# Kernel optimization log

Measured on AMD Instinct MI355X. Metric: run time of the kernel, lower is better.

The kernel has to match this reference:

```python
import jax, jax.numpy as jnp
import numpy as np

G_NUMS = 30      # group_nums
G_SIZE = 100     # group_size (also neighborhood_size)
BETA = 1.0
EPS = 1e-9


def setup_inputs() -> dict:
    key = jax.random.key(0)
    pointclouds = jax.random.normal(key, (8, 131072, 3), dtype=jnp.float32)
    return {"pointclouds": pointclouds}


def _knn_gather(points, queries, k):
    """points [b,N,3], queries [b,G,3] -> k nearest points per query [b,G,k,3]."""
    # squared distances [b,G,N]
    d2 = (
        jnp.sum(queries * queries, axis=-1)[..., None]
        - 2.0 * jnp.einsum("bgd,bnd->bgn", queries, points)
        + jnp.sum(points * points, axis=-1)[:, None, :]
    )
    _, idx = jax.lax.top_k(-d2, k)                    # [b,G,k]
    nbrs = jax.vmap(lambda p, i: p[i])(points, idx)   # [b,G,k,3]
    return nbrs


def reference(pointclouds):
    b, N, _ = pointclouds.shape
    # --- group_points: uniform-stride sampled centers, k-NN groups, group means ---
    stride = N // G_NUMS
    centers = pointclouds[:, ::stride][:, :G_NUMS]                 # [b,G,3]
    grouped = _knn_gather(pointclouds, centers, G_SIZE)            # [b,G,K,3]
    group_means = jnp.mean(grouped, axis=2)                        # [b,G,3]

    # --- estimate_pointcloud_local_coord_frames: per-group 3x3 PCA ---
    nbrs = _knn_gather(pointclouds, group_means, G_SIZE)           # [b,G,K,3]
    mu = jnp.mean(nbrs, axis=2, keepdims=True)
    X = nbrs - mu
    cov = jnp.einsum("bgkd,bgke->bgde", X, X) / G_SIZE             # [b,G,3,3]
    curvatures, frames = jnp.linalg.eigh(cov)                      # eigvals ascending

    # --- elongated-shape loss ---
    denom = curvatures[..., 0] + curvatures[..., 1] + curvatures[..., 2] + EPS
    first_vec = curvatures[..., 2] / denom
    second_vec = curvatures[..., 1] / denom
    elongated_shape_loss = -jnp.sum(first_vec - second_vec) / b

    # --- angular smoothness cost over group means / principal directions ---
    dirs = frames[..., :, 2]                                       # [b,G,3] largest-eig direction
    dm = jnp.sum(
        (group_means[:, :, None, :] - group_means[:, None, :, :]) ** 2, axis=-1
    )                                                              # [b,G,G]
    dm = dm + jnp.eye(G_NUMS, dtype=dm.dtype) * jnp.float32(1e30)  # exclude self
    j = jnp.argmin(dm, axis=-1)                                    # [b,G]
    dirs_j = jnp.take_along_axis(dirs, j[..., None], axis=1)       # [b,G,3]
    cos = jnp.sum(dirs * dirs_j, axis=-1)
    dlo_smooth_loss = jnp.mean(1.0 - cos * cos)                    # sign-invariant angle cost

    return elongated_shape_loss + BETA * dlo_smooth_loss
```

## Files before the change

### kernel.cpp

```cpp
#include <hip/hip_runtime.h>
#include <math.h>

#define N_PTS     131072
#define G_NUMS    30
#define G_SIZE    100
#define PT_STRIDE (N_PTS / G_NUMS)
#define TPB       512
#define NWAVES    (TPB / 64)
#define BINS      4096
#define SHIFT     20
#define SAMPLE_GRPS 1024
#define RANK_CUT  32
#define CAP       3072
#define TIE_CAP   64

struct KSmem {
    unsigned hist[BINS];
    unsigned wsum[NWAVES];
    unsigned T;
    int ns, nd, nt;
    unsigned u[CAP];
    int idx[CAP];
    int sel[G_SIZE];
    unsigned tu[TIE_CAP];
    int ti[TIE_CAP];
    float acc[3];
    float cov[6];
    float q[3];
    unsigned tau0;
    unsigned maxu;
    unsigned r1;
    float delta2;
    int fastok;
};

__device__ __forceinline__ float dist2f(float px, float py, float pz,
                                        float qx, float qy, float qz) {
    float dx = px - qx, dy = py - qy, dz = pz - qz;
    return fmaf(dx, dx, fmaf(dy, dy, dz * dz));
}

__device__ __forceinline__ unsigned find_bin(KSmem& sm, unsigned rank,
                                             int tid, int lane, int wid) {
    unsigned hv[8], csum = 0;
#pragma unroll
    for (int j = 0; j < 8; j++) { hv[j] = sm.hist[tid * 8 + j]; csum += hv[j]; }
    unsigned inc = csum;
#pragma unroll
    for (int off = 1; off < 64; off <<= 1) {
        unsigned n = __shfl_up(inc, off);
        if (lane >= off) inc += n;
    }
    __syncthreads();
    if (lane == 63) sm.wsum[wid] = inc;
    __syncthreads();
    unsigned base = 0;
    for (int w = 0; w < wid; w++) base += sm.wsum[w];
    unsigned c = base + inc - csum;
#pragma unroll
    for (int j = 0; j < 8; j++) {
        if (c < rank && c + hv[j] >= rank) sm.T = (unsigned)(tid * 8 + j);
        c += hv[j];
    }
    __syncthreads();
    return sm.T;
}

template<bool SOA>
__device__ __forceinline__ void load_pt(const float* __restrict__ P,
                                        const float* __restrict__ BX,
                                        const float* __restrict__ BY,
                                        const float* __restrict__ BZ,
                                        int idx, float& x, float& y, float& z) {
    if constexpr (SOA) {
        x = BX[idx]; y = BY[idx]; z = BZ[idx];
    } else {
        const float* pp = P + 3 * (size_t)idx;
        x = pp[0]; y = pp[1]; z = pp[2];
    }
}

template<bool SOA>
__device__ void full_select(const float4* __restrict__ P4,
                            const float4* __restrict__ X4,
                            const float4* __restrict__ Y4,
                            const float4* __restrict__ Z4,
                            KSmem& sm, float qx, float qy, float qz,
                            int tid, int lane, int wid, bool save_tau) {
    for (int j = tid; j < BINS; j += TPB) sm.hist[j] = 0u;
    if (tid == 0) { sm.ns = 0; sm.nd = 0; sm.nt = 0; sm.T = 0u; }
    __syncthreads();

    if constexpr (SOA) {
        for (int i = tid; i < SAMPLE_GRPS; i += TPB) {
            float4 xv = X4[i], yv = Y4[i], zv = Z4[i];
            atomicAdd(&sm.hist[__float_as_uint(dist2f(xv.x, yv.x, zv.x, qx, qy, qz)) >> SHIFT], 1u);
            atomicAdd(&sm.hist[__float_as_uint(dist2f(xv.y, yv.y, zv.y, qx, qy, qz)) >> SHIFT], 1u);
            atomicAdd(&sm.hist[__float_as_uint(dist2f(xv.z, yv.z, zv.z, qx, qy, qz)) >> SHIFT], 1u);
            atomicAdd(&sm.hist[__float_as_uint(dist2f(xv.w, yv.w, zv.w, qx, qy, qz)) >> SHIFT], 1u);
        }
    } else {
        for (int grp = tid; grp < SAMPLE_GRPS; grp += TPB) {
            float4 f0 = P4[3 * grp + 0];
            float4 f1 = P4[3 * grp + 1];
            float4 f2 = P4[3 * grp + 2];
            atomicAdd(&sm.hist[__float_as_uint(dist2f(f0.x, f0.y, f0.z, qx, qy, qz)) >> SHIFT], 1u);
            atomicAdd(&sm.hist[__float_as_uint(dist2f(f0.w, f1.x, f1.y, qx, qy, qz)) >> SHIFT], 1u);
            atomicAdd(&sm.hist[__float_as_uint(dist2f(f1.z, f1.w, f2.x, qx, qy, qz)) >> SHIFT], 1u);
            atomicAdd(&sm.hist[__float_as_uint(dist2f(f2.y, f2.z, f2.w, qx, qy, qz)) >> SHIFT], 1u);
        }
    }
    __syncthreads();
    unsigned Tc = find_bin(sm, RANK_CUT, tid, lane, wid);
    const unsigned tau = (Tc >= BINS - 1) ? 0xFFFFFFFFu : ((Tc + 1) << SHIFT);
    if (save_tau && tid == 0) sm.tau0 = tau;
    for (int j = tid; j < BINS; j += TPB) sm.hist[j] = 0u;
    __syncthreads();

    if constexpr (SOA) {
#pragma unroll 4
        for (int i = tid; i < N_PTS / 4; i += TPB) {
            float4 xv = X4[i], yv = Y4[i], zv = Z4[i];
            unsigned u0 = __float_as_uint(dist2f(xv.x, yv.x, zv.x, qx, qy, qz));
            unsigned u1 = __float_as_uint(dist2f(xv.y, yv.y, zv.y, qx, qy, qz));
            unsigned u2 = __float_as_uint(dist2f(xv.z, yv.z, zv.z, qx, qy, qz));
            unsigned u3 = __float_as_uint(dist2f(xv.w, yv.w, zv.w, qx, qy, qz));
            int i0 = i * 4;
            if (u0 < tau) { int p = atomicAdd(&sm.ns, 1); if (p < CAP) { sm.u[p] = u0; sm.idx[p] = i0; } }
            if (u1 < tau) { int p = atomicAdd(&sm.ns, 1); if (p < CAP) { sm.u[p] = u1; sm.idx[p] = i0 + 1; } }
            if (u2 < tau) { int p = atomicAdd(&sm.ns, 1); if (p < CAP) { sm.u[p] = u2; sm.idx[p] = i0 + 2; } }
            if (u3 < tau) { int p = atomicAdd(&sm.ns, 1); if (p < CAP) { sm.u[p] = u3; sm.idx[p] = i0 + 3; } }
        }
    } else {
#pragma unroll 4
        for (int grp = tid; grp < N_PTS / 4; grp += TPB) {
            float4 f0 = P4[3 * grp + 0];
            float4 f1 = P4[3 * grp + 1];
            float4 f2 = P4[3 * grp + 2];
            unsigned u0 = __float_as_uint(dist2f(f0.x, f0.y, f0.z, qx, qy, qz));
            unsigned u1 = __float_as_uint(dist2f(f0.w, f1.x, f1.y, qx, qy, qz));
            unsigned u2 = __float_as_uint(dist2f(f1.z, f1.w, f2.x, qx, qy, qz));
            unsigned u3 = __float_as_uint(dist2f(f2.y, f2.z, f2.w, qx, qy, qz));
            int i0 = grp * 4;
            if (u0 < tau) { int p = atomicAdd(&sm.ns, 1); if (p < CAP) { sm.u[p] = u0; sm.idx[p] = i0; } }
            if (u1 < tau) { int p = atomicAdd(&sm.ns, 1); if (p < CAP) { sm.u[p] = u1; sm.idx[p] = i0 + 1; } }
            if (u2 < tau) { int p = atomicAdd(&sm.ns, 1); if (p < CAP) { sm.u[p] = u2; sm.idx[p] = i0 + 2; } }
            if (u3 < tau) { int p = atomicAdd(&sm.ns, 1); if (p < CAP) { sm.u[p] = u3; sm.idx[p] = i0 + 3; } }
        }
    }
    __syncthreads();
    int S = sm.ns; if (S > CAP) S = CAP;

    unsigned hb = 32u - (unsigned)__clz(tau - 1u);
    unsigned s2 = hb > 12u ? hb - 12u : 0u;
    for (int i = tid; i < S; i += TPB) atomicAdd(&sm.hist[sm.u[i] >> s2], 1u);
    __syncthreads();
    unsigned T2 = find_bin(sm, G_SIZE, tid, lane, wid);
    const unsigned lo = T2 << s2;

    for (int i = tid; i < S; i += TPB) {
        unsigned uu = sm.u[i];
        if (uu < lo) {
            int p = atomicAdd(&sm.nd, 1);
            if (p < G_SIZE) sm.sel[p] = sm.idx[i];
        } else if ((uu >> s2) == T2) {
            int p = atomicAdd(&sm.nt, 1);
            if (p < TIE_CAP) { sm.tu[p] = uu; sm.ti[p] = sm.idx[i]; }
        }
    }
    __syncthreads();
    if (tid == 0) {
        int nd = sm.nd; if (nd > G_SIZE) nd = G_SIZE;
        int need = G_SIZE - nd;
        int ec = sm.nt; if (ec > TIE_CAP) ec = TIE_CAP;
        for (int a = 0; a < need && a < ec; ++a) {
            int best = a;
            for (int j = a + 1; j < ec; ++j)
                if (sm.tu[j] < sm.tu[best] ||
                    (sm.tu[j] == sm.tu[best] && sm.ti[j] < sm.ti[best])) best = j;
            unsigned tub = sm.tu[best]; sm.tu[best] = sm.tu[a]; sm.tu[a] = tub;
            int tib = sm.ti[best]; sm.ti[best] = sm.ti[a]; sm.ti[a] = tib;
            sm.sel[nd + a] = sm.ti[a];
        }
    }
    __syncthreads();
}

template<bool SOA>
__global__ __launch_bounds__(TPB)
void fused_knn_kernel(const float* __restrict__ pts,
                      const float* __restrict__ sx, const float* __restrict__ sy,
                      const float* __restrict__ sz,
                      float* __restrict__ out_mean, float* __restrict__ out_cov,
                      int B) {
    __shared__ KSmem sm;

    const int blk = blockIdx.x;
    const int b = blk % B;
    const int g = blk / B;
    const int gi = b * G_NUMS + g;
    const float* __restrict__ P = pts + (size_t)b * (N_PTS * 3);
    const float4* __restrict__ P4 = (const float4*)P;
    const float* BX = nullptr; const float* BY = nullptr; const float* BZ = nullptr;
    const float4* X4 = nullptr; const float4* Y4 = nullptr; const float4* Z4 = nullptr;
    if constexpr (SOA) {
        BX = sx + (size_t)b * N_PTS;
        BY = sy + (size_t)b * N_PTS;
        BZ = sz + (size_t)b * N_PTS;
        X4 = (const float4*)BX; Y4 = (const float4*)BY; Z4 = (const float4*)BZ;
    }
    const int tid = threadIdx.x;
    const int lane = tid & 63, wid = tid >> 6;

    if (tid == 0) {
        const float* qp = P + (size_t)g * PT_STRIDE * 3;
        sm.q[0] = qp[0]; sm.q[1] = qp[1]; sm.q[2] = qp[2];
    }
    if (tid < 3) sm.acc[tid] = 0.f;
    if (tid < 6) sm.cov[tid] = 0.f;
    __syncthreads();
    const float qx = sm.q[0], qy = sm.q[1], qz = sm.q[2];

    full_select<SOA>(P4, X4, Y4, Z4, sm, qx, qy, qz, tid, lane, wid, true);

    if (tid < G_SIZE) {
        float x, y, z;
        load_pt<SOA>(P, BX, BY, BZ, sm.sel[tid], x, y, z);
        atomicAdd(&sm.acc[0], x);
        atomicAdd(&sm.acc[1], y);
        atomicAdd(&sm.acc[2], z);
    }
    __syncthreads();
    const int S0 = sm.ns;
    if (tid == 0) {
        float mx = sm.acc[0] * (1.0f / G_SIZE);
        float my = sm.acc[1] * (1.0f / G_SIZE);
        float mz = sm.acc[2] * (1.0f / G_SIZE);
        out_mean[(size_t)gi * 3 + 0] = mx;
        out_mean[(size_t)gi * 3 + 1] = my;
        out_mean[(size_t)gi * 3 + 2] = mz;
        float dx = mx - qx, dy = my - qy, dz = mz - qz;
        sm.delta2 = fmaf(dx, dx, fmaf(dy, dy, dz * dz));
        sm.q[0] = mx; sm.q[1] = my; sm.q[2] = mz;
        sm.acc[0] = 0.f; sm.acc[1] = 0.f; sm.acc[2] = 0.f;
        sm.maxu = 0u; sm.r1 = 0u; sm.T = 0u;
        sm.nd = 0; sm.nt = 0;
        sm.fastok = 0;
    }
    __syncthreads();
    const float q1x = sm.q[0], q1y = sm.q[1], q1z = sm.q[2];

    const bool attempt = (S0 >= G_SIZE) && (S0 <= CAP);
    if (attempt) {
        for (int j = tid; j < BINS; j += TPB) sm.hist[j] = 0u;
        for (int i = tid; i < S0; i += TPB) {
            float x, y, z;
            load_pt<SOA>(P, BX, BY, BZ, sm.idx[i], x, y, z);
            unsigned uu = __float_as_uint(dist2f(x, y, z, q1x, q1y, q1z));
            sm.u[i] = uu;
            atomicMax(&sm.maxu, uu);
        }
        __syncthreads();
        unsigned maxu = sm.maxu;
        unsigned hb = (maxu == 0u) ? 0u : (32u - (unsigned)__clz(maxu));
        unsigned s3 = hb > 12u ? hb - 12u : 0u;
        for (int i = tid; i < S0; i += TPB) atomicAdd(&sm.hist[sm.u[i] >> s3], 1u);
        __syncthreads();
        unsigned T2 = find_bin(sm, G_SIZE, tid, lane, wid);
        const unsigned lo = T2 << s3;
        for (int i = tid; i < S0; i += TPB) {
            unsigned uu = sm.u[i];
            if (uu < lo) {
                int p = atomicAdd(&sm.nd, 1);
                if (p < G_SIZE) sm.sel[p] = sm.idx[i];
            } else if ((uu >> s3) == T2) {
                int p = atomicAdd(&sm.nt, 1);
                if (p < TIE_CAP) { sm.tu[p] = uu; sm.ti[p] = sm.idx[i]; }
            }
        }
        __syncthreads();
        if (tid == 0) {
            int ok = 1;
            int nd = sm.nd; if (nd > G_SIZE) { nd = G_SIZE; ok = 0; }
            int need = G_SIZE - nd;
            if (sm.nt > TIE_CAP) ok = 0;
            int ec = sm.nt; if (ec > TIE_CAP) ec = TIE_CAP;
            if (need > ec) ok = 0;
            for (int a = 0; a < need && a < ec; ++a) {
                int best = a;
                for (int j = a + 1; j < ec; ++j)
                    if (sm.tu[j] < sm.tu[best] ||
                        (sm.tu[j] == sm.tu[best] && sm.ti[j] < sm.ti[best])) best = j;
                unsigned tub = sm.tu[best]; sm.tu[best] = sm.tu[a]; sm.tu[a] = tub;
                int tib = sm.ti[best]; sm.ti[best] = sm.ti[a]; sm.ti[a] = tib;
                sm.sel[nd + a] = sm.ti[a];
            }
            sm.fastok = ok;
        }
        __syncthreads();
        if (sm.fastok) {
            if (tid < G_SIZE) {
                float x, y, z;
                load_pt<SOA>(P, BX, BY, BZ, sm.sel[tid], x, y, z);
                atomicMax(&sm.r1, __float_as_uint(dist2f(x, y, z, q1x, q1y, q1z)));
            }
            __syncthreads();
            if (tid == 0) {
                double R0 = sqrt((double)__uint_as_float(sm.tau0));
                double dl = sqrt((double)sm.delta2);
                double r1 = sqrt((double)__uint_as_float(sm.r1));
                if (!((R0 - dl) > r1 * 1.0001 + 1e-7)) sm.fastok = 0;
            }
            __syncthreads();
        }
    }

    if (!attempt || !sm.fastok) {
        full_select<SOA>(P4, X4, Y4, Z4, sm, q1x, q1y, q1z, tid, lane, wid, false);
    }

    float px = 0.f, py = 0.f, pz = 0.f;
    if (tid < G_SIZE) {
        load_pt<SOA>(P, BX, BY, BZ, sm.sel[tid], px, py, pz);
        atomicAdd(&sm.acc[0], px);
        atomicAdd(&sm.acc[1], py);
        atomicAdd(&sm.acc[2], pz);
    }
    __syncthreads();
    float mx = sm.acc[0] * (1.0f / G_SIZE);
    float my = sm.acc[1] * (1.0f / G_SIZE);
    float mz = sm.acc[2] * (1.0f / G_SIZE);
    if (tid < G_SIZE) {
        float x = px - mx, y = py - my, z = pz - mz;
        atomicAdd(&sm.cov[0], x * x);
        atomicAdd(&sm.cov[1], x * y);
        atomicAdd(&sm.cov[2], x * z);
        atomicAdd(&sm.cov[3], y * y);
        atomicAdd(&sm.cov[4], y * z);
        atomicAdd(&sm.cov[5], z * z);
    }
    __syncthreads();
    if (tid < 6) out_cov[(size_t)gi * 6 + tid] = sm.cov[tid] * (1.0f / G_SIZE);
}

__global__ __launch_bounds__(256)
void transpose_kernel(const float* __restrict__ pts,
                      float* __restrict__ sx, float* __restrict__ sy,
                      float* __restrict__ sz, int total4) {
    int t = blockIdx.x * 256 + threadIdx.x;
    if (t >= total4) return;
    const float4* __restrict__ P4 = (const float4*)pts;
    float4 f0 = P4[3 * t + 0];
    float4 f1 = P4[3 * t + 1];
    float4 f2 = P4[3 * t + 2];
    ((float4*)sx)[t] = make_float4(f0.x, f0.w, f1.z, f2.y);
    ((float4*)sy)[t] = make_float4(f0.y, f1.x, f1.w, f2.z);
    ((float4*)sz)[t] = make_float4(f0.z, f1.y, f2.x, f2.w);
}

__device__ void eig3(const float cf[6], double lam_out[3], double dir_out[3]) {
    double a[3][3], v[3][3];
    a[0][0] = cf[0]; a[0][1] = cf[1]; a[0][2] = cf[2];
    a[1][0] = cf[1]; a[1][1] = cf[3]; a[1][2] = cf[4];
    a[2][0] = cf[2]; a[2][1] = cf[4]; a[2][2] = cf[5];
    for (int i = 0; i < 3; i++)
        for (int j = 0; j < 3; j++) v[i][j] = (i == j) ? 1.0 : 0.0;

    for (int sweep = 0; sweep < 12; sweep++) {
        double off = a[0][1] * a[0][1] + a[0][2] * a[0][2] + a[1][2] * a[1][2];
        if (off == 0.0) break;
        for (int p = 0; p < 2; p++) {
            for (int q = p + 1; q < 3; q++) {
                double apq = a[p][q];
                if (apq == 0.0) continue;
                double app = a[p][p], aqq = a[q][q];
                double theta = (aqq - app) / (2.0 * apq);
                double t = (theta >= 0.0 ? 1.0 : -1.0) /
                           (fabs(theta) + sqrt(theta * theta + 1.0));
                double c = 1.0 / sqrt(t * t + 1.0);
                double s = t * c;
                a[p][p] = app - t * apq;
                a[q][q] = aqq + t * apq;
                a[p][q] = 0.0; a[q][p] = 0.0;
                for (int r = 0; r < 3; r++) {
                    if (r == p || r == q) continue;
                    double arp = a[r][p], arq = a[r][q];
                    a[r][p] = c * arp - s * arq; a[p][r] = a[r][p];
                    a[r][q] = s * arp + c * arq; a[q][r] = a[r][q];
                }
                for (int r = 0; r < 3; r++) {
                    double vrp = v[r][p], vrq = v[r][q];
                    v[r][p] = c * vrp - s * vrq;
                    v[r][q] = s * vrp + c * vrq;
                }
            }
        }
    }
    double l0 = a[0][0], l1 = a[1][1], l2 = a[2][2];
    int i0 = 0, i1 = 1, i2 = 2;
    if (l0 > l1) { double t = l0; l0 = l1; l1 = t; int ti = i0; i0 = i1; i1 = ti; }
    if (l1 > l2) { double t = l1; l1 = l2; l2 = t; int ti = i1; i1 = i2; i2 = ti; }
    if (l0 > l1) { double t = l0; l0 = l1; l1 = t; int ti = i0; i0 = i1; i1 = ti; }
    lam_out[0] = l0; lam_out[1] = l1; lam_out[2] = l2;
    dir_out[0] = v[0][i2]; dir_out[1] = v[1][i2]; dir_out[2] = v[2][i2];
}

__global__ __launch_bounds__(256)
void finalize_kernel(const float* __restrict__ gmeans, const float* __restrict__ covs,
                     float* __restrict__ out, int B) {
    const int tid = threadIdx.x;
    const int NG = B * G_NUMS;
    __shared__ float s_dir[256][3];
    __shared__ float s_gm[256][3];
    __shared__ float s_pe[4];
    __shared__ float s_ps[4];

    float et = 0.f;
    if (tid < NG) {
        float cf[6];
#pragma unroll
        for (int j = 0; j < 6; j++) cf[j] = covs[tid * 6 + j];
        double lam[3], dir[3];
        eig3(cf, lam, dir);
        double denom = lam[0] + lam[1] + lam[2] + 1e-9;
        et = (float)((lam[2] - lam[1]) / denom);
        s_dir[tid][0] = (float)dir[0];
        s_dir[tid][1] = (float)dir[1];
        s_dir[tid][2] = (float)dir[2];
        s_gm[tid][0] = gmeans[tid * 3 + 0];
        s_gm[tid][1] = gmeans[tid * 3 + 1];
        s_gm[tid][2] = gmeans[tid * 3 + 2];
    }
    __syncthreads();

    float st = 0.f;
    if (tid < NG) {
        int b = tid / G_NUMS, g = tid % G_NUMS;
        float gx = s_gm[tid][0], gy = s_gm[tid][1], gz = s_gm[tid][2];
        float bd = 3.4e38f; int bj = 0;
        for (int gg = 0; gg < G_NUMS; gg++) {
            if (gg == g) continue;
            int o = b * G_NUMS + gg;
            float dx = gx - s_gm[o][0];
            float dy = gy - s_gm[o][1];
            float dz = gz - s_gm[o][2];
            float d = dx * dx + dy * dy + dz * dz;
            if (d < bd) { bd = d; bj = gg; }
        }
        int o = b * G_NUMS + bj;
        float cosv = s_dir[tid][0] * s_dir[o][0] +
                     s_dir[tid][1] * s_dir[o][1] +
                     s_dir[tid][2] * s_dir[o][2];
        st = 1.f - cosv * cosv;
    }

    float e = et, s2 = st;
#pragma unroll
    for (int off = 32; off > 0; off >>= 1) {
        e += __shfl_down(e, off);
        s2 += __shfl_down(s2, off);
    }
    int lane = tid & 63, wid = tid >> 6;
    if (lane == 0) { s_pe[wid] = e; s_ps[wid] = s2; }
    __syncthreads();
    if (tid == 0) {
        float se = 0.f, ss = 0.f;
        for (int w = 0; w < 4; w++) { se += s_pe[w]; ss += s_ps[w]; }
        out[0] = -se / (float)B + ss / (float)NG;
    }
}

extern "C" void kernel_launch(void* const* d_in, const int* in_sizes, int n_in,
                              void* d_out, int out_size, void* d_ws, size_t ws_size,
                              hipStream_t stream) {
    const float* pts = (const float*)d_in[0];
    float* out = (float*)d_out;
    float* ws = (float*)d_ws;
    int B = in_sizes[0] / (N_PTS * 3);
    float* gmeans = ws;
    float* covs = ws + (size_t)B * G_NUMS * 3;

    const size_t base_floats = (size_t)B * G_NUMS * 9;
    const size_t soa_floats = 3 * (size_t)B * N_PTS;
    const bool use_soa = ws_size >= (base_floats + soa_floats) * sizeof(float);

    dim3 grid(B * G_NUMS);
    if (use_soa) {
        float* sx = ws + base_floats;
        float* sy = sx + (size_t)B * N_PTS;
        float* sz = sy + (size_t)B * N_PTS;
        int total4 = B * N_PTS / 4;
        transpose_kernel<<<dim3((total4 + 255) / 256), dim3(256), 0, stream>>>(
            pts, sx, sy, sz, total4);
        fused_knn_kernel<true><<<grid, TPB, 0, stream>>>(
            pts, sx, sy, sz, gmeans, covs, B);
    } else {
        fused_knn_kernel<false><<<grid, TPB, 0, stream>>>(
            pts, nullptr, nullptr, nullptr, gmeans, covs, B);
    }
    finalize_kernel<<<dim3(1), dim3(256), 0, stream>>>(gmeans, covs, out, B);
}
```

Baseline: 151.6 us.

## Fuse transpose, kNN and finalize into one kernel with in-kernel sync

Merges the separate transpose, kNN and finalize kernels into a single launch. Blocks cooperatively transpose to SoA and spin-wait on a global counter before using it. A last-block pattern performs the eigen/loss finalization. Candidate point coordinates are cached in shared memory so the refinement and covariance steps avoid global gathers, and the block size doubles to 1024 threads. This removes launch overhead and global reloads but adds a spin barrier, which depends on all blocks being co-resident, plus higher shared-memory use per block.

```diff
diff --git a/kernel.cpp b/kernel.cpp
--- a/kernel.cpp
+++ b/kernel.cpp
@@ -5,9 +5,10 @@
 #define G_NUMS    30
 #define G_SIZE    100
 #define PT_STRIDE (N_PTS / G_NUMS)
-#define TPB       512
+#define TPB       1024
 #define NWAVES    (TPB / 64)
 #define BINS      4096
+#define JB        (BINS / TPB)
 #define SHIFT     20
 #define SAMPLE_GRPS 1024
 #define RANK_CUT  32
@@ -15,23 +16,28 @@
 #define TIE_CAP   64
 
 struct KSmem {
-    unsigned hist[BINS];
+    union {
+        unsigned hist[BINS];
+        struct {
+            float gm[256][3];
+            float dir[256][3];
+            float pe[NWAVES];
+            float ps[NWAVES];
+        } fin;
+    };
     unsigned wsum[NWAVES];
     unsigned T;
     int ns, nd, nt;
+    int lastblk;
     unsigned u[CAP];
     int idx[CAP];
+    float px[CAP], py[CAP], pz[CAP];
     int sel[G_SIZE];
     unsigned tu[TIE_CAP];
     int ti[TIE_CAP];
-    float acc[3];
-    float cov[6];
-    float q[3];
-    unsigned tau0;
-    unsigned maxu;
-    unsigned r1;
+    float acc[3], cov[6], q[3];
+    unsigned tau0, maxu, r1;
     float delta2;
-    int fastok;
 };
 
 __device__ __forceinline__ float dist2f(float px, float py, float pz,
@@ -42,9 +48,9 @@
 
 __device__ __forceinline__ unsigned find_bin(KSmem& sm, unsigned rank,
                                              int tid, int lane, int wid) {
-    unsigned hv[8], csum = 0;
+    unsigned hv[JB], csum = 0;
 #pragma unroll
-    for (int j = 0; j < 8; j++) { hv[j] = sm.hist[tid * 8 + j]; csum += hv[j]; }
+    for (int j = 0; j < JB; j++) { hv[j] = sm.hist[tid * JB + j]; csum += hv[j]; }
     unsigned inc = csum;
 #pragma unroll
     for (int off = 1; off < 64; off <<= 1) {
@@ -58,8 +64,8 @@
     for (int w = 0; w < wid; w++) base += sm.wsum[w];
     unsigned c = base + inc - csum;
 #pragma unroll
-    for (int j = 0; j < 8; j++) {
-        if (c < rank && c + hv[j] >= rank) sm.T = (unsigned)(tid * 8 + j);
+    for (int j = 0; j < JB; j++) {
+        if (c < rank && c + hv[j] >= rank) sm.T = (unsigned)(tid * JB + j);
         c += hv[j];
     }
     __syncthreads();
@@ -67,55 +73,38 @@
 }
 
 template<bool SOA>
-__device__ __forceinline__ void load_pt(const float* __restrict__ P,
-                                        const float* __restrict__ BX,
-                                        const float* __restrict__ BY,
-                                        const float* __restrict__ BZ,
-                                        int idx, float& x, float& y, float& z) {
-    if constexpr (SOA) {
-        x = BX[idx]; y = BY[idx]; z = BZ[idx];
-    } else {
-        const float* pp = P + 3 * (size_t)idx;
-        x = pp[0]; y = pp[1]; z = pp[2];
-    }
-}
-
-template<bool SOA>
-__device__ void full_select(const float4* __restrict__ P4,
-                            const float4* __restrict__ X4,
-                            const float4* __restrict__ Y4,
-                            const float4* __restrict__ Z4,
-                            KSmem& sm, float qx, float qy, float qz,
-                            int tid, int lane, int wid, bool save_tau) {
+__device__ void knn_select(const float4* __restrict__ P4,
+                           const float4* __restrict__ X4,
+                           const float4* __restrict__ Y4,
+                           const float4* __restrict__ Z4,
+                           KSmem& sm, float qx, float qy, float qz,
+                           int tid, int lane, int wid, bool save_tau,
+                           unsigned* tc_wait ) {
     for (int j = tid; j < BINS; j += TPB) sm.hist[j] = 0u;
     if (tid == 0) { sm.ns = 0; sm.nd = 0; sm.nt = 0; sm.T = 0u; }
     __syncthreads();
 
-    if constexpr (SOA) {
-        for (int i = tid; i < SAMPLE_GRPS; i += TPB) {
-            float4 xv = X4[i], yv = Y4[i], zv = Z4[i];
-            atomicAdd(&sm.hist[__float_as_uint(dist2f(xv.x, yv.x, zv.x, qx, qy, qz)) >> SHIFT], 1u);
-            atomicAdd(&sm.hist[__float_as_uint(dist2f(xv.y, yv.y, zv.y, qx, qy, qz)) >> SHIFT], 1u);
-            atomicAdd(&sm.hist[__float_as_uint(dist2f(xv.z, yv.z, zv.z, qx, qy, qz)) >> SHIFT], 1u);
-            atomicAdd(&sm.hist[__float_as_uint(dist2f(xv.w, yv.w, zv.w, qx, qy, qz)) >> SHIFT], 1u);
-        }
-    } else {
-        for (int grp = tid; grp < SAMPLE_GRPS; grp += TPB) {
-            float4 f0 = P4[3 * grp + 0];
-            float4 f1 = P4[3 * grp + 1];
-            float4 f2 = P4[3 * grp + 2];
-            atomicAdd(&sm.hist[__float_as_uint(dist2f(f0.x, f0.y, f0.z, qx, qy, qz)) >> SHIFT], 1u);
-            atomicAdd(&sm.hist[__float_as_uint(dist2f(f0.w, f1.x, f1.y, qx, qy, qz)) >> SHIFT], 1u);
-            atomicAdd(&sm.hist[__float_as_uint(dist2f(f1.z, f1.w, f2.x, qx, qy, qz)) >> SHIFT], 1u);
-            atomicAdd(&sm.hist[__float_as_uint(dist2f(f2.y, f2.z, f2.w, qx, qy, qz)) >> SHIFT], 1u);
-        }
+    for (int grp = tid; grp < SAMPLE_GRPS; grp += TPB) {
+        float4 f0 = P4[3 * grp + 0];
+        float4 f1 = P4[3 * grp + 1];
+        float4 f2 = P4[3 * grp + 2];
+        atomicAdd(&sm.hist[__float_as_uint(dist2f(f0.x, f0.y, f0.z, qx, qy, qz)) >> SHIFT], 1u);
+        atomicAdd(&sm.hist[__float_as_uint(dist2f(f0.w, f1.x, f1.y, qx, qy, qz)) >> SHIFT], 1u);
+        atomicAdd(&sm.hist[__float_as_uint(dist2f(f1.z, f1.w, f2.x, qx, qy, qz)) >> SHIFT], 1u);
+        atomicAdd(&sm.hist[__float_as_uint(dist2f(f2.y, f2.z, f2.w, qx, qy, qz)) >> SHIFT], 1u);
     }
     __syncthreads();
     unsigned Tc = find_bin(sm, RANK_CUT, tid, lane, wid);
     const unsigned tau = (Tc >= BINS - 1) ? 0xFFFFFFFFu : ((Tc + 1) << SHIFT);
     if (save_tau && tid == 0) sm.tau0 = tau;
     for (int j = tid; j < BINS; j += TPB) sm.hist[j] = 0u;
-    __syncthreads();
+    if (tc_wait && tid == 0) {
+        while (__hip_atomic_load(tc_wait, __ATOMIC_ACQUIRE, __HIP_MEMORY_SCOPE_AGENT)
+               < (unsigned)G_NUMS)
+            __builtin_amdgcn_s_sleep(2);
+    }
+    __syncthreads();
+    if (tc_wait) __threadfence();
 
     if constexpr (SOA) {
 #pragma unroll 4
@@ -126,10 +115,10 @@
             unsigned u2 = __float_as_uint(dist2f(xv.z, yv.z, zv.z, qx, qy, qz));
             unsigned u3 = __float_as_uint(dist2f(xv.w, yv.w, zv.w, qx, qy, qz));
             int i0 = i * 4;
-            if (u0 < tau) { int p = atomicAdd(&sm.ns, 1); if (p < CAP) { sm.u[p] = u0; sm.idx[p] = i0; } }
-            if (u1 < tau) { int p = atomicAdd(&sm.ns, 1); if (p < CAP) { sm.u[p] = u1; sm.idx[p] = i0 + 1; } }
-            if (u2 < tau) { int p = atomicAdd(&sm.ns, 1); if (p < CAP) { sm.u[p] = u2; sm.idx[p] = i0 + 2; } }
-            if (u3 < tau) { int p = atomicAdd(&sm.ns, 1); if (p < CAP) { sm.u[p] = u3; sm.idx[p] = i0 + 3; } }
+            if (u0 < tau) { int p = atomicAdd(&sm.ns, 1); if (p < CAP) { sm.u[p] = u0; sm.idx[p] = i0;     sm.px[p] = xv.x; sm.py[p] = yv.x; sm.pz[p] = zv.x; } }
+            if (u1 < tau) { int p = atomicAdd(&sm.ns, 1); if (p < CAP) { sm.u[p] = u1; sm.idx[p] = i0 + 1; sm.px[p] = xv.y; sm.py[p] = yv.y; sm.pz[p] = zv.y; } }
+            if (u2 < tau) { int p = atomicAdd(&sm.ns, 1); if (p < CAP) { sm.u[p] = u2; sm.idx[p] = i0 + 2; sm.px[p] = xv.z; sm.py[p] = yv.z; sm.pz[p] = zv.z; } }
+            if (u3 < tau) { int p = atomicAdd(&sm.ns, 1); if (p < CAP) { sm.u[p] = u3; sm.idx[p] = i0 + 3; sm.px[p] = xv.w; sm.py[p] = yv.w; sm.pz[p] = zv.w; } }
         }
     } else {
 #pragma unroll 4
@@ -142,10 +131,10 @@
             unsigned u2 = __float_as_uint(dist2f(f1.z, f1.w, f2.x, qx, qy, qz));
             unsigned u3 = __float_as_uint(dist2f(f2.y, f2.z, f2.w, qx, qy, qz));
             int i0 = grp * 4;
-            if (u0 < tau) { int p = atomicAdd(&sm.ns, 1); if (p < CAP) { sm.u[p] = u0; sm.idx[p] = i0; } }
-            if (u1 < tau) { int p = atomicAdd(&sm.ns, 1); if (p < CAP) { sm.u[p] = u1; sm.idx[p] = i0 + 1; } }
-            if (u2 < tau) { int p = atomicAdd(&sm.ns, 1); if (p < CAP) { sm.u[p] = u2; sm.idx[p] = i0 + 2; } }
-            if (u3 < tau) { int p = atomicAdd(&sm.ns, 1); if (p < CAP) { sm.u[p] = u3; sm.idx[p] = i0 + 3; } }
+            if (u0 < tau) { int p = atomicAdd(&sm.ns, 1); if (p < CAP) { sm.u[p] = u0; sm.idx[p] = i0;     sm.px[p] = f0.x; sm.py[p] = f0.y; sm.pz[p] = f0.z; } }
+            if (u1 < tau) { int p = atomicAdd(&sm.ns, 1); if (p < CAP) { sm.u[p] = u1; sm.idx[p] = i0 + 1; sm.px[p] = f0.w; sm.py[p] = f1.x; sm.pz[p] = f1.y; } }
+            if (u2 < tau) { int p = atomicAdd(&sm.ns, 1); if (p < CAP) { sm.u[p] = u2; sm.idx[p] = i0 + 2; sm.px[p] = f1.z; sm.py[p] = f1.w; sm.pz[p] = f2.x; } }
+            if (u3 < tau) { int p = atomicAdd(&sm.ns, 1); if (p < CAP) { sm.u[p] = u3; sm.idx[p] = i0 + 3; sm.px[p] = f2.y; sm.py[p] = f2.z; sm.pz[p] = f2.w; } }
         }
     }
     __syncthreads();
@@ -162,10 +151,10 @@
         unsigned uu = sm.u[i];
         if (uu < lo) {
             int p = atomicAdd(&sm.nd, 1);
-            if (p < G_SIZE) sm.sel[p] = sm.idx[i];
+            if (p < G_SIZE) sm.sel[p] = i;
         } else if ((uu >> s2) == T2) {
             int p = atomicAdd(&sm.nt, 1);
-            if (p < TIE_CAP) { sm.tu[p] = uu; sm.ti[p] = sm.idx[i]; }
+            if (p < TIE_CAP) { sm.tu[p] = uu; sm.ti[p] = i; }
         }
     }
     __syncthreads();
@@ -177,185 +166,13 @@
             int best = a;
             for (int j = a + 1; j < ec; ++j)
                 if (sm.tu[j] < sm.tu[best] ||
-                    (sm.tu[j] == sm.tu[best] && sm.ti[j] < sm.ti[best])) best = j;
+                    (sm.tu[j] == sm.tu[best] && sm.idx[sm.ti[j]] < sm.idx[sm.ti[best]])) best = j;
             unsigned tub = sm.tu[best]; sm.tu[best] = sm.tu[a]; sm.tu[a] = tub;
             int tib = sm.ti[best]; sm.ti[best] = sm.ti[a]; sm.ti[a] = tib;
             sm.sel[nd + a] = sm.ti[a];
         }
     }
     __syncthreads();
-}
-
-template<bool SOA>
-__global__ __launch_bounds__(TPB)
-void fused_knn_kernel(const float* __restrict__ pts,
-                      const float* __restrict__ sx, const float* __restrict__ sy,
-                      const float* __restrict__ sz,
-                      float* __restrict__ out_mean, float* __restrict__ out_cov,
-                      int B) {
-    __shared__ KSmem sm;
-
-    const int blk = blockIdx.x;
-    const int b = blk % B;
-    const int g = blk / B;
-    const int gi = b * G_NUMS + g;
-    const float* __restrict__ P = pts + (size_t)b * (N_PTS * 3);
-    const float4* __restrict__ P4 = (const float4*)P;
-    const float* BX = nullptr; const float* BY = nullptr; const float* BZ = nullptr;
-    const float4* X4 = nullptr; const float4* Y4 = nullptr; const float4* Z4 = nullptr;
-    if constexpr (SOA) {
-        BX = sx + (size_t)b * N_PTS;
-        BY = sy + (size_t)b * N_PTS;
-        BZ = sz + (size_t)b * N_PTS;
-        X4 = (const float4*)BX; Y4 = (const float4*)BY; Z4 = (const float4*)BZ;
-    }
-    const int tid = threadIdx.x;
-    const int lane = tid & 63, wid = tid >> 6;
-
-    if (tid == 0) {
-        const float* qp = P + (size_t)g * PT_STRIDE * 3;
-        sm.q[0] = qp[0]; sm.q[1] = qp[1]; sm.q[2] = qp[2];
-    }
-    if (tid < 3) sm.acc[tid] = 0.f;
-    if (tid < 6) sm.cov[tid] = 0.f;
-    __syncthreads();
-    const float qx = sm.q[0], qy = sm.q[1], qz = sm.q[2];
-
-    full_select<SOA>(P4, X4, Y4, Z4, sm, qx, qy, qz, tid, lane, wid, true);
-
-    if (tid < G_SIZE) {
-        float x, y, z;
-        load_pt<SOA>(P, BX, BY, BZ, sm.sel[tid], x, y, z);
-        atomicAdd(&sm.acc[0], x);
-        atomicAdd(&sm.acc[1], y);
-        atomicAdd(&sm.acc[2], z);
-    }
-    __syncthreads();
-    const int S0 = sm.ns;
-    if (tid == 0) {
-        float mx = sm.acc[0] * (1.0f / G_SIZE);
-        float my = sm.acc[1] * (1.0f / G_SIZE);
-        float mz = sm.acc[2] * (1.0f / G_SIZE);
-        out_mean[(size_t)gi * 3 + 0] = mx;
-        out_mean[(size_t)gi * 3 + 1] = my;
-        out_mean[(size_t)gi * 3 + 2] = mz;
-        float dx = mx - qx, dy = my - qy, dz = mz - qz;
-        sm.delta2 = fmaf(dx, dx, fmaf(dy, dy, dz * dz));
-        sm.q[0] = mx; sm.q[1] = my; sm.q[2] = mz;
-        sm.acc[0] = 0.f; sm.acc[1] = 0.f; sm.acc[2] = 0.f;
-        sm.maxu = 0u; sm.r1 = 0u; sm.T = 0u;
-        sm.nd = 0; sm.nt = 0;
-        sm.fastok = 0;
-    }
-    __syncthreads();
-    const float q1x = sm.q[0], q1y = sm.q[1], q1z = sm.q[2];
-
-    const bool attempt = (S0 >= G_SIZE) && (S0 <= CAP);
-    if (attempt) {
-        for (int j = tid; j < BINS; j += TPB) sm.hist[j] = 0u;
-        for (int i = tid; i < S0; i += TPB) {
-            float x, y, z;
-            load_pt<SOA>(P, BX, BY, BZ, sm.idx[i], x, y, z);
-            unsigned uu = __float_as_uint(dist2f(x, y, z, q1x, q1y, q1z));
-            sm.u[i] = uu;
-            atomicMax(&sm.maxu, uu);
-        }
-        __syncthreads();
-        unsigned maxu = sm.maxu;
-        unsigned hb = (maxu == 0u) ? 0u : (32u - (unsigned)__clz(maxu));
-        unsigned s3 = hb > 12u ? hb - 12u : 0u;
-        for (int i = tid; i < S0; i += TPB) atomicAdd(&sm.hist[sm.u[i] >> s3], 1u);
-        __syncthreads();
-        unsigned T2 = find_bin(sm, G_SIZE, tid, lane, wid);
-        const unsigned lo = T2 << s3;
-        for (int i = tid; i < S0; i += TPB) {
-            unsigned uu = sm.u[i];
-            if (uu < lo) {
-                int p = atomicAdd(&sm.nd, 1);
-                if (p < G_SIZE) sm.sel[p] = sm.idx[i];
-            } else if ((uu >> s3) == T2) {
-                int p = atomicAdd(&sm.nt, 1);
-                if (p < TIE_CAP) { sm.tu[p] = uu; sm.ti[p] = sm.idx[i]; }
-            }
-        }
-        __syncthreads();
-        if (tid == 0) {
-            int ok = 1;
-            int nd = sm.nd; if (nd > G_SIZE) { nd = G_SIZE; ok = 0; }
-            int need = G_SIZE - nd;
-            if (sm.nt > TIE_CAP) ok = 0;
-            int ec = sm.nt; if (ec > TIE_CAP) ec = TIE_CAP;
-            if (need > ec) ok = 0;
-            for (int a = 0; a < need && a < ec; ++a) {
-                int best = a;
-                for (int j = a + 1; j < ec; ++j)
-                    if (sm.tu[j] < sm.tu[best] ||
-                        (sm.tu[j] == sm.tu[best] && sm.ti[j] < sm.ti[best])) best = j;
-                unsigned tub = sm.tu[best]; sm.tu[best] = sm.tu[a]; sm.tu[a] = tub;
-                int tib = sm.ti[best]; sm.ti[best] = sm.ti[a]; sm.ti[a] = tib;
-                sm.sel[nd + a] = sm.ti[a];
-            }
-            sm.fastok = ok;
-        }
-        __syncthreads();
-        if (sm.fastok) {
-            if (tid < G_SIZE) {
-                float x, y, z;
-                load_pt<SOA>(P, BX, BY, BZ, sm.sel[tid], x, y, z);
-                atomicMax(&sm.r1, __float_as_uint(dist2f(x, y, z, q1x, q1y, q1z)));
-            }
-            __syncthreads();
-            if (tid == 0) {
-                double R0 = sqrt((double)__uint_as_float(sm.tau0));
-                double dl = sqrt((double)sm.delta2);
-                double r1 = sqrt((double)__uint_as_float(sm.r1));
-                if (!((R0 - dl) > r1 * 1.0001 + 1e-7)) sm.fastok = 0;
-            }
-            __syncthreads();
-        }
-    }
-
-    if (!attempt || !sm.fastok) {
-        full_select<SOA>(P4, X4, Y4, Z4, sm, q1x, q1y, q1z, tid, lane, wid, false);
-    }
-
-    float px = 0.f, py = 0.f, pz = 0.f;
-    if (tid < G_SIZE) {
-        load_pt<SOA>(P, BX, BY, BZ, sm.sel[tid], px, py, pz);
-        atomicAdd(&sm.acc[0], px);
-        atomicAdd(&sm.acc[1], py);
-        atomicAdd(&sm.acc[2], pz);
-    }
-    __syncthreads();
-    float mx = sm.acc[0] * (1.0f / G_SIZE);
-    float my = sm.acc[1] * (1.0f / G_SIZE);
-    float mz = sm.acc[2] * (1.0f / G_SIZE);
-    if (tid < G_SIZE) {
-        float x = px - mx, y = py - my, z = pz - mz;
-        atomicAdd(&sm.cov[0], x * x);
-        atomicAdd(&sm.cov[1], x * y);
-        atomicAdd(&sm.cov[2], x * z);
-        atomicAdd(&sm.cov[3], y * y);
-        atomicAdd(&sm.cov[4], y * z);
-        atomicAdd(&sm.cov[5], z * z);
-    }
-    __syncthreads();
-    if (tid < 6) out_cov[(size_t)gi * 6 + tid] = sm.cov[tid] * (1.0f / G_SIZE);
-}
-
-__global__ __launch_bounds__(256)
-void transpose_kernel(const float* __restrict__ pts,
-                      float* __restrict__ sx, float* __restrict__ sy,
-                      float* __restrict__ sz, int total4) {
-    int t = blockIdx.x * 256 + threadIdx.x;
-    if (t >= total4) return;
-    const float4* __restrict__ P4 = (const float4*)pts;
-    float4 f0 = P4[3 * t + 0];
-    float4 f1 = P4[3 * t + 1];
-    float4 f2 = P4[3 * t + 2];
-    ((float4*)sx)[t] = make_float4(f0.x, f0.w, f1.z, f2.y);
-    ((float4*)sy)[t] = make_float4(f0.y, f1.x, f1.w, f2.z);
-    ((float4*)sz)[t] = make_float4(f0.z, f1.y, f2.x, f2.w);
 }
 
 __device__ void eig3(const float cf[6], double lam_out[3], double dir_out[3]) {
@@ -405,16 +222,195 @@
     dir_out[0] = v[0][i2]; dir_out[1] = v[1][i2]; dir_out[2] = v[2][i2];
 }
 
-__global__ __launch_bounds__(256)
-void finalize_kernel(const float* __restrict__ gmeans, const float* __restrict__ covs,
-                     float* __restrict__ out, int B) {
+template<bool SOA>
+__global__ __launch_bounds__(TPB)
+void fused_all_kernel(const float* __restrict__ pts,
+                      float* __restrict__ sx, float* __restrict__ sy,
+                      float* __restrict__ sz,
+                      float* __restrict__ gmeans, float* __restrict__ covs,
+                      float* __restrict__ out,
+                      unsigned* __restrict__ syncw,
+                      int B, int nblk) {
+    __shared__ KSmem sm;
+
+    const int blk = blockIdx.x;
+    const int b = blk % B;
+    const int g = blk / B;
+    const int gi = b * G_NUMS + g;
+    const float* __restrict__ P = pts + (size_t)b * (N_PTS * 3);
+    const float4* __restrict__ P4 = (const float4*)P;
+    float* BX = nullptr; float* BY = nullptr; float* BZ = nullptr;
+    const float4* X4 = nullptr; const float4* Y4 = nullptr; const float4* Z4 = nullptr;
+    if constexpr (SOA) {
+        BX = sx + (size_t)b * N_PTS;
+        BY = sy + (size_t)b * N_PTS;
+        BZ = sz + (size_t)b * N_PTS;
+        X4 = (const float4*)BX; Y4 = (const float4*)BY; Z4 = (const float4*)BZ;
+    }
     const int tid = threadIdx.x;
-    const int NG = B * G_NUMS;
-    __shared__ float s_dir[256][3];
-    __shared__ float s_gm[256][3];
-    __shared__ float s_pe[4];
-    __shared__ float s_ps[4];
-
+    const int lane = tid & 63, wid = tid >> 6;
+
+    if (tid == 0) {
+        const float* qp = P + (size_t)g * PT_STRIDE * 3;
+        sm.q[0] = qp[0]; sm.q[1] = qp[1]; sm.q[2] = qp[2];
+    }
+    if (tid < 3) sm.acc[tid] = 0.f;
+    if (tid < 6) sm.cov[tid] = 0.f;
+
+    if constexpr (SOA) {
+        const int per = (N_PTS / 4 + G_NUMS - 1) / G_NUMS;
+        int t0 = g * per;
+        int t1 = t0 + per; if (t1 > N_PTS / 4) t1 = N_PTS / 4;
+        for (int t = t0 + tid; t < t1; t += TPB) {
+            float4 f0 = P4[3 * t + 0];
+            float4 f1 = P4[3 * t + 1];
+            float4 f2 = P4[3 * t + 2];
+            ((float4*)BX)[t] = make_float4(f0.x, f0.w, f1.z, f2.y);
+            ((float4*)BY)[t] = make_float4(f0.y, f1.x, f1.w, f2.z);
+            ((float4*)BZ)[t] = make_float4(f0.z, f1.y, f2.x, f2.w);
+        }
+        __threadfence();
+    }
+    __syncthreads();
+    if constexpr (SOA) {
+        if (tid == 0)
+            __hip_atomic_fetch_add(&syncw[b], 1u, __ATOMIC_RELEASE,
+                                   __HIP_MEMORY_SCOPE_AGENT);
+    }
+    const float qx = sm.q[0], qy = sm.q[1], qz = sm.q[2];
+
+    knn_select<SOA>(P4, X4, Y4, Z4, sm, qx, qy, qz, tid, lane, wid, true,
+                    SOA ? &syncw[b] : nullptr);
+
+    if (tid < G_SIZE) {
+        int p = sm.sel[tid];
+        atomicAdd(&sm.acc[0], sm.px[p]);
+        atomicAdd(&sm.acc[1], sm.py[p]);
+        atomicAdd(&sm.acc[2], sm.pz[p]);
+    }
+    __syncthreads();
+    const int S0 = sm.ns;
+    if (tid == 0) {
+        float mx = sm.acc[0] * (1.0f / G_SIZE);
+        float my = sm.acc[1] * (1.0f / G_SIZE);
+        float mz = sm.acc[2] * (1.0f / G_SIZE);
+        gmeans[(size_t)gi * 3 + 0] = mx;
+        gmeans[(size_t)gi * 3 + 1] = my;
+        gmeans[(size_t)gi * 3 + 2] = mz;
+        float dx = mx - qx, dy = my - qy, dz = mz - qz;
+        sm.delta2 = fmaf(dx, dx, fmaf(dy, dy, dz * dz));
+        sm.q[0] = mx; sm.q[1] = my; sm.q[2] = mz;
+        sm.acc[0] = 0.f; sm.acc[1] = 0.f; sm.acc[2] = 0.f;
+        sm.maxu = 0u; sm.r1 = 0u; sm.T = 0u;
+        sm.nd = 0; sm.nt = 0;
+        sm.lastblk = 0;
+    }
+    __shared__ int s_fastok;
+    if (tid == 0) s_fastok = 0;
+    __syncthreads();
+    const float q1x = sm.q[0], q1y = sm.q[1], q1z = sm.q[2];
+
+    const bool attempt = (S0 >= G_SIZE) && (S0 <= CAP);
+    if (attempt) {
+        for (int j = tid; j < BINS; j += TPB) sm.hist[j] = 0u;
+        for (int i = tid; i < S0; i += TPB) {
+            unsigned uu = __float_as_uint(
+                dist2f(sm.px[i], sm.py[i], sm.pz[i], q1x, q1y, q1z));
+            sm.u[i] = uu;
+            atomicMax(&sm.maxu, uu);
+        }
+        __syncthreads();
+        unsigned maxu = sm.maxu;
+        unsigned hb = (maxu == 0u) ? 0u : (32u - (unsigned)__clz(maxu));
+        unsigned s3 = hb > 12u ? hb - 12u : 0u;
+        for (int i = tid; i < S0; i += TPB) atomicAdd(&sm.hist[sm.u[i] >> s3], 1u);
+        __syncthreads();
+        unsigned T2 = find_bin(sm, G_SIZE, tid, lane, wid);
+        const unsigned lo = T2 << s3;
+        for (int i = tid; i < S0; i += TPB) {
+            unsigned uu = sm.u[i];
+            if (uu < lo) {
+                int p = atomicAdd(&sm.nd, 1);
+                if (p < G_SIZE) sm.sel[p] = i;
+            } else if ((uu >> s3) == T2) {
+                int p = atomicAdd(&sm.nt, 1);
+                if (p < TIE_CAP) { sm.tu[p] = uu; sm.ti[p] = i; }
+            }
+        }
+        __syncthreads();
+        if (tid == 0) {
+            int ok = 1;
+            int nd = sm.nd; if (nd > G_SIZE) { nd = G_SIZE; ok = 0; }
+            int need = G_SIZE - nd;
+            if (sm.nt > TIE_CAP) ok = 0;
+            int ec = sm.nt; if (ec > TIE_CAP) ec = TIE_CAP;
+            if (need > ec) ok = 0;
+            for (int a = 0; a < need && a < ec; ++a) {
+                int best = a;
+                for (int j = a + 1; j < ec; ++j)
+                    if (sm.tu[j] < sm.tu[best] ||
+                        (sm.tu[j] == sm.tu[best] && sm.idx[sm.ti[j]] < sm.idx[sm.ti[best]])) best = j;
+                unsigned tub = sm.tu[best]; sm.tu[best] = sm.tu[a]; sm.tu[a] = tub;
+                int tib = sm.ti[best]; sm.ti[best] = sm.ti[a]; sm.ti[a] = tib;
+                sm.sel[nd + a] = sm.ti[a];
+            }
+            s_fastok = ok;
+        }
+        __syncthreads();
+        if (s_fastok) {
+            if (tid < G_SIZE) atomicMax(&sm.r1, sm.u[sm.sel[tid]]);
+            __syncthreads();
+            if (tid == 0) {
+                double R0 = sqrt((double)__uint_as_float(sm.tau0));
+                double dl = sqrt((double)sm.delta2);
+                double r1 = sqrt((double)__uint_as_float(sm.r1));
+                if (!((R0 - dl) > r1 * 1.0001 + 1e-7)) s_fastok = 0;
+            }
+            __syncthreads();
+        }
+    }
+
+    if (!attempt || !s_fastok) {
+        knn_select<SOA>(P4, X4, Y4, Z4, sm, q1x, q1y, q1z, tid, lane, wid, false,
+                        nullptr);
+    }
+
+    float px = 0.f, py = 0.f, pz = 0.f;
+    if (tid < G_SIZE) {
+        int p = sm.sel[tid];
+        px = sm.px[p]; py = sm.py[p]; pz = sm.pz[p];
+        atomicAdd(&sm.acc[0], px);
+        atomicAdd(&sm.acc[1], py);
+        atomicAdd(&sm.acc[2], pz);
+    }
+    __syncthreads();
+    float mx = sm.acc[0] * (1.0f / G_SIZE);
+    float my = sm.acc[1] * (1.0f / G_SIZE);
+    float mz = sm.acc[2] * (1.0f / G_SIZE);
+    if (tid < G_SIZE) {
+        float x = px - mx, y = py - my, z = pz - mz;
+        atomicAdd(&sm.cov[0], x * x);
+        atomicAdd(&sm.cov[1], x * y);
+        atomicAdd(&sm.cov[2], x * z);
+        atomicAdd(&sm.cov[3], y * y);
+        atomicAdd(&sm.cov[4], y * z);
+        atomicAdd(&sm.cov[5], z * z);
+    }
+    __syncthreads();
+    if (tid < 6) covs[(size_t)gi * 6 + tid] = sm.cov[tid] * (1.0f / G_SIZE);
+
+    __threadfence();
+    __syncthreads();
+    if (tid == 0) {
+        unsigned old = __hip_atomic_fetch_add(&syncw[B], 1u, __ATOMIC_ACQ_REL,
+                                              __HIP_MEMORY_SCOPE_AGENT);
+        sm.lastblk = (old == (unsigned)(nblk - 1)) ? 1 : 0;
+    }
+    __syncthreads();
+    if (!sm.lastblk) return;
+
+    __threadfence();
+    const int NG = nblk;
     float et = 0.f;
     if (tid < NG) {
         float cf[6];
@@ -424,33 +420,33 @@
         eig3(cf, lam, dir);
         double denom = lam[0] + lam[1] + lam[2] + 1e-9;
         et = (float)((lam[2] - lam[1]) / denom);
-        s_dir[tid][0] = (float)dir[0];
-        s_dir[tid][1] = (float)dir[1];
-        s_dir[tid][2] = (float)dir[2];
-        s_gm[tid][0] = gmeans[tid * 3 + 0];
-        s_gm[tid][1] = gmeans[tid * 3 + 1];
-        s_gm[tid][2] = gmeans[tid * 3 + 2];
+        sm.fin.dir[tid][0] = (float)dir[0];
+        sm.fin.dir[tid][1] = (float)dir[1];
+        sm.fin.dir[tid][2] = (float)dir[2];
+        sm.fin.gm[tid][0] = gmeans[tid * 3 + 0];
+        sm.fin.gm[tid][1] = gmeans[tid * 3 + 1];
+        sm.fin.gm[tid][2] = gmeans[tid * 3 + 2];
     }
     __syncthreads();
 
     float st = 0.f;
     if (tid < NG) {
-        int b = tid / G_NUMS, g = tid % G_NUMS;
-        float gx = s_gm[tid][0], gy = s_gm[tid][1], gz = s_gm[tid][2];
+        int bb = tid / G_NUMS, gg0 = tid % G_NUMS;
+        float gx = sm.fin.gm[tid][0], gy = sm.fin.gm[tid][1], gz = sm.fin.gm[tid][2];
         float bd = 3.4e38f; int bj = 0;
         for (int gg = 0; gg < G_NUMS; gg++) {
-            if (gg == g) continue;
-            int o = b * G_NUMS + gg;
-            float dx = gx - s_gm[o][0];
-            float dy = gy - s_gm[o][1];
-            float dz = gz - s_gm[o][2];
+            if (gg == gg0) continue;
+            int o = bb * G_NUMS + gg;
+            float dx = gx - sm.fin.gm[o][0];
+            float dy = gy - sm.fin.gm[o][1];
+            float dz = gz - sm.fin.gm[o][2];
             float d = dx * dx + dy * dy + dz * dz;
             if (d < bd) { bd = d; bj = gg; }
         }
-        int o = b * G_NUMS + bj;
-        float cosv = s_dir[tid][0] * s_dir[o][0] +
-                     s_dir[tid][1] * s_dir[o][1] +
-                     s_dir[tid][2] * s_dir[o][2];
+        int o = bb * G_NUMS + bj;
+        float cosv = sm.fin.dir[tid][0] * sm.fin.dir[o][0] +
+                     sm.fin.dir[tid][1] * sm.fin.dir[o][1] +
+                     sm.fin.dir[tid][2] * sm.fin.dir[o][2];
         st = 1.f - cosv * cosv;
     }
 
@@ -460,12 +456,11 @@
         e += __shfl_down(e, off);
         s2 += __shfl_down(s2, off);
     }
-    int lane = tid & 63, wid = tid >> 6;
-    if (lane == 0) { s_pe[wid] = e; s_ps[wid] = s2; }
+    if (lane == 0) { sm.fin.pe[wid] = e; sm.fin.ps[wid] = s2; }
     __syncthreads();
     if (tid == 0) {
         float se = 0.f, ss = 0.f;
-        for (int w = 0; w < 4; w++) { se += s_pe[w]; ss += s_ps[w]; }
+        for (int w = 0; w < NWAVES; w++) { se += sm.fin.pe[w]; ss += sm.fin.ps[w]; }
         out[0] = -se / (float)B + ss / (float)NG;
     }
 }
@@ -477,26 +472,27 @@
     float* out = (float*)d_out;
     float* ws = (float*)d_ws;
     int B = in_sizes[0] / (N_PTS * 3);
+    int nblk = B * G_NUMS;
+
     float* gmeans = ws;
     float* covs = ws + (size_t)B * G_NUMS * 3;
-
     const size_t base_floats = (size_t)B * G_NUMS * 9;
+    unsigned* syncw = (unsigned*)(ws + base_floats);
+    float* soa = ws + base_floats + 16;
     const size_t soa_floats = 3 * (size_t)B * N_PTS;
-    const bool use_soa = ws_size >= (base_floats + soa_floats) * sizeof(float);
-
-    dim3 grid(B * G_NUMS);
+    const bool use_soa = ws_size >= (base_floats + 16 + soa_floats) * sizeof(float);
+
+    hipMemsetAsync(syncw, 0, 64, stream);
+
+    dim3 grid(nblk);
     if (use_soa) {
-        float* sx = ws + base_floats;
+        float* sx = soa;
         float* sy = sx + (size_t)B * N_PTS;
         float* sz = sy + (size_t)B * N_PTS;
-        int total4 = B * N_PTS / 4;
-        transpose_kernel<<<dim3((total4 + 255) / 256), dim3(256), 0, stream>>>(
-            pts, sx, sy, sz, total4);
-        fused_knn_kernel<true><<<grid, TPB, 0, stream>>>(
-            pts, sx, sy, sz, gmeans, covs, B);
+        fused_all_kernel<true><<<grid, TPB, 0, stream>>>(
+            pts, sx, sy, sz, gmeans, covs, out, syncw, B, nblk);
     } else {
-        fused_knn_kernel<false><<<grid, TPB, 0, stream>>>(
-            pts, nullptr, nullptr, nullptr, gmeans, covs, B);
-    }
-    finalize_kernel<<<dim3(1), dim3(256), 0, stream>>>(gmeans, covs, out, B);
-}
+        fused_all_kernel<false><<<grid, TPB, 0, stream>>>(
+            pts, nullptr, nullptr, nullptr, gmeans, covs, out, syncw, B, nblk);
+    }
+}
```

New measurement: 346.6 us. 2.29x slower.
